# Kernel optimization log

Measured on AMD Instinct MI355X. Metric: run time of the kernel, lower is better.

The kernel has to match this reference:

```python
import jax, jax.numpy as jnp
import numpy as np

GAMMA = 0.03125  # 1/D
REG = 1e-3


def rbf_gram(X, Y, gamma):
    # avoiding the naive [N, M, D] diff tensor from the torch source.
    xx = jnp.sum(X * X, axis=-1)  # [N]
    yy = jnp.sum(Y * Y, axis=-1)  # [M]
    sq = xx[:, None] + yy[None, :] - 2.0 * (X @ Y.T)  # [N, M]
    sq = jnp.maximum(sq, 0.0)
    return jnp.exp(-gamma * sq)


def setup_inputs() -> dict:
    key = jax.random.key(0)
    k1, k2, k3 = jax.random.split(key, 3)
    N, M, D = 8192, 8192, 32
    X_train = jax.random.normal(k1, (N, D), dtype=jnp.float32)
    y_train = jax.random.normal(k2, (N,), dtype=jnp.float32)
    X_test = jax.random.normal(k3, (M, D), dtype=jnp.float32)
    return {"X_train": X_train, "y_train": y_train, "X_test": X_test}


def reference(X_train, y_train, X_test):
    # fit: solve (K + reg * I) alpha = y
    N = X_train.shape[0]
    K = rbf_gram(X_train, X_train, GAMMA)  # [N, N]
    A = K + REG * jnp.eye(N, dtype=K.dtype)
    alpha = jnp.linalg.solve(A, y_train[:, None])[:, 0]  # [N]
    # predict: K_test @ alpha
    K_test = rbf_gram(X_test, X_train, GAMMA)  # [M, N]
    return K_test @ alpha  # [M]
```

## Files before the change

### kernel.cpp

```cpp
#include <hip/hip_runtime.h>


#define NN 8192
#define DD 32
#define REGL 1e-3f
#define NITER 96
#define NBLK 256
#define NC2 (-0.045084220027780106f)
#define SCF (0.3002806023f)

typedef short v8s __attribute__((ext_vector_type(8)));
typedef float v4f __attribute__((ext_vector_type(4)));

__device__ __forceinline__ float fast_exp2(float x) {
#if __has_builtin(__builtin_amdgcn_exp2f)
  return __builtin_amdgcn_exp2f(x);
#else
  float r;
  asm("v_exp_f32 %0, %1" : "=v"(r) : "v"(x));
  return r;
#endif
}

__device__ __forceinline__ float ld_f(const float* p) {
  return __hip_atomic_load(p, __ATOMIC_RELAXED, __HIP_MEMORY_SCOPE_AGENT);
}
__device__ __forceinline__ void st_f(float* p, float v) {
  __hip_atomic_store(p, v, __ATOMIC_RELAXED, __HIP_MEMORY_SCOPE_AGENT);
}
__device__ __forceinline__ double ld_d(const double* p) {
  return __hip_atomic_load(p, __ATOMIC_RELAXED, __HIP_MEMORY_SCOPE_AGENT);
}
__device__ __forceinline__ void st_d(double* p, double v) {
  __hip_atomic_store(p, v, __ATOMIC_RELAXED, __HIP_MEMORY_SCOPE_AGENT);
}

__device__ __forceinline__ ushort f2bf(float x) {
  unsigned u = __float_as_uint(x);
  return (ushort)((u + 0x7fff + ((u >> 16) & 1)) >> 16);
}
__device__ __forceinline__ float bf2f(ushort b) {
  return __uint_as_float(((unsigned)b) << 16);
}

__device__ __forceinline__ double bfly64_d(double v) {
#pragma unroll
  for (int m = 1; m < 64; m <<= 1) v += __shfl_xor(v, m, 64);
  return v;
}
__device__ __forceinline__ double wave_down_sum_d(double v) {
#pragma unroll
  for (int off = 32; off > 0; off >>= 1) v += __shfl_down(v, off, 64);
  return v;
}

__device__ __forceinline__ void gbarrier(unsigned* bar) {
  __builtin_amdgcn_s_waitcnt(0);
  __syncthreads();
  if (threadIdx.x == 0) {
    unsigned* gen = bar + 272;
    unsigned g =
        __hip_atomic_load(gen, __ATOMIC_RELAXED, __HIP_MEMORY_SCOPE_AGENT);
    unsigned a = __hip_atomic_fetch_add(&bar[(blockIdx.x >> 4) * 16], 1u,
                                        __ATOMIC_RELAXED,
                                        __HIP_MEMORY_SCOPE_AGENT);
    bool pub = false;
    if (a == 15u) {
      unsigned ra = __hip_atomic_fetch_add(bar + 256, 1u, __ATOMIC_RELAXED,
                                           __HIP_MEMORY_SCOPE_AGENT);
      if (ra == 15u) {
#pragma unroll
        for (int k = 0; k < 16; ++k)
          __hip_atomic_store(&bar[k * 16], 0u, __ATOMIC_RELAXED,
                             __HIP_MEMORY_SCOPE_AGENT);
        __hip_atomic_store(bar + 256, 0u, __ATOMIC_RELAXED,
                           __HIP_MEMORY_SCOPE_AGENT);
        __builtin_amdgcn_s_waitcnt(0);
        __hip_atomic_store(gen, g + 1u, __ATOMIC_RELAXED,
                           __HIP_MEMORY_SCOPE_AGENT);
        pub = true;
      }
    }
    if (!pub) {
      unsigned t = 0;
      while (__hip_atomic_load(gen, __ATOMIC_RELAXED,
                               __HIP_MEMORY_SCOPE_AGENT) == g) {
        if (t < 64)
          __builtin_amdgcn_s_sleep(1);
        else
          __builtin_amdgcn_s_sleep(8);
        if (++t > (1u << 20)) break;
      }
    }
  }
  __atomic_signal_fence(__ATOMIC_SEQ_CST);
  __syncthreads();
}

__device__ __forceinline__ void conv_frag(const float* __restrict__ X, int row,
                                          int kb, v8s& h, v8s& l) {
  const float4* rp = (const float4*)(X + (size_t)row * DD + kb);
  float4 f0 = rp[0], f1 = rp[1];
  float f[8] = {f0.x, f0.y, f0.z, f0.w, f1.x, f1.y, f1.z, f1.w};
  union {
    v8s v;
    ushort u[8];
  } H, L;
#pragma unroll
  for (int j = 0; j < 8; ++j) {
    float fs = SCF * f[j];
    ushort hb = f2bf(fs);
    H.u[j] = hb;
    L.u[j] = f2bf(fs - bf2f(hb));
  }
  h = H.v;
  l = L.v;
}


__global__ void setup_zero(unsigned* __restrict__ bar) {
  int i = blockIdx.x * 256 + threadIdx.x;
  if (i < 512) bar[i] = 0u;
}

__global__ void row_norms(const float* __restrict__ X, float* __restrict__ xx) {
  int i = blockIdx.x * blockDim.x + threadIdx.x;
  if (i < NN) {
    const float4* row = (const float4*)(X + (size_t)i * DD);
    float s = 0.f;
#pragma unroll
    for (int k = 0; k < DD / 4; ++k) {
      float4 v = row[k];
      s += v.x * v.x + v.y * v.y + v.z * v.z + v.w * v.w;
    }
    xx[i] = NC2 * s;
  }
}

__device__ __forceinline__ void mv_compute(const v8s* ah, const v8s* al,
                                           const ushort (*Bh)[512],
                                           const ushort (*Bl)[512],
                                           const float* Wj, int lane,
                                           float racc[4][4]) {
  const int n = lane & 15;
  for (int t = 0; t < 16; ++t) {
    v8s bh = *(const v8s*)&Bh[t][lane * 8];
    v8s bl = *(const v8s*)&Bl[t][lane * 8];
    float wn = Wj[t * 16 + n];
#pragma unroll
    for (int rs = 0; rs < 4; ++rs) {
      v4f c = {0.f, 0.f, 0.f, 0.f};
      c = __builtin_amdgcn_mfma_f32_16x16x32_bf16(al[rs], bh, c, 0, 0, 0);
      c = __builtin_amdgcn_mfma_f32_16x16x32_bf16(ah[rs], bl, c, 0, 0, 0);
      c = __builtin_amdgcn_mfma_f32_16x16x32_bf16(ah[rs], bh, c, 0, 0, 0);
#pragma unroll
      for (int u = 0; u < 4; ++u)
        racc[rs][u] = fmaf(fast_exp2(c[u]), wn, racc[rs][u]);
    }
  }
}


__global__ __launch_bounds__(1024, 4) void cg_persist(
    const float* __restrict__ Xtr, const float* __restrict__ Xte,
    const float* __restrict__ xx_tr, const float* __restrict__ xx_te,
    const float* __restrict__ y, float* __restrict__ qp0,
    float* __restrict__ qp1, double* __restrict__ rho_s,
    double* __restrict__ mu_s, unsigned* __restrict__ bar,
    float* __restrict__ out, int db) {
  __shared__ __align__(16) ushort Bh[16][512];
  __shared__ __align__(16) ushort Bl[16][512];
  __shared__ float Wj[256];
  __shared__ float Ebj[256];
  __shared__ float Erow[1024];
  __shared__ float Rrow[1024], Qrow[1024];
  __shared__ float Rcol[256], Qcol[256], Pcol[256], Xcol[256];
  __shared__ double sredq[16];
  __shared__ double sredr[16];
  __shared__ float s_ab[2];

  const int tid = threadIdx.x;
  const int lane = tid & 63;
  const int wid = tid >> 6;
  const int n = lane & 15, q4 = lane >> 4;
  const int rbi = blockIdx.x & 7;
  const int sli = blockIdx.x >> 3;
  const int rowbase = rbi * 1024;
  const int i0 = rowbase + wid * 64;
  const int jbase = sli * 256;

  {
    int c = tid & 255;
    int j = jbase + c;
    int g = tid >> 8;
    int tile = c >> 4, cl = c & 15;
    const float4* rp = (const float4*)(Xtr + (size_t)j * DD);
    float4 f0 = rp[2 * g], f1 = rp[2 * g + 1];
    float f[8] = {f0.x, f0.y, f0.z, f0.w, f1.x, f1.y, f1.z, f1.w};
    union {
      ushort u[8];
      uint4 qq;
    } H, L;
#pragma unroll
    for (int e = 0; e < 8; ++e) {
      float fs = SCF * f[e];
      ushort hb = f2bf(fs);
      H.u[e] = hb;
      L.u[e] = f2bf(fs - bf2f(hb));
    }
    int ln = cl + 16 * g;
    *(uint4*)&Bh[tile][ln * 8] = H.qq;
    *(uint4*)&Bl[tile][ln * 8] = L.qq;
  }
  if (tid < 256) Ebj[tid] = fast_exp2(xx_tr[jbase + tid]);
  Erow[tid] = fast_exp2(xx_tr[rowbase + tid]);

  Rrow[tid] = y[rowbase + tid];
  Qrow[tid] = 0.f;
  if (tid < 256) {
    Rcol[tid] = y[jbase + tid];
    Qcol[tid] = 0.f;
    Pcol[tid] = 0.f;
    Xcol[tid] = 0.f;
  }

  v8s ah[4], al[4];
#pragma unroll
  for (int rs = 0; rs < 4; ++rs)
    conv_frag(Xtr, i0 + rs * 16 + n, q4 * 8, ah[rs], al[rs]);

  double rho_old = 1.0, alpha_old = 1.0;
  __syncthreads();

  for (int it = 0; it < NITER; ++it) {
    float* qp = (db && (it & 1)) ? qp1 : qp0;

    if (tid < 256) Wj[tid] = Rcol[tid] * Ebj[tid];
    if (sli == 0) {
      float rvv = Rrow[tid];
      double acc = wave_down_sum_d((double)rvv * (double)rvv);
      if (lane == 0) sredr[wid] = acc;
    }
    __syncthreads();
    if (sli == 0 && tid == 0) {
      double t = 0.0;
#pragma unroll
      for (int k3 = 0; k3 < 16; ++k3) t += sredr[k3];
      st_d(&rho_s[(size_t)it * 128 + rbi * 16], t);
    }

    float racc[4][4] = {};
    mv_compute(ah, al, Bh, Bl, Wj, lane, racc);
#pragma unroll
    for (int rs = 0; rs < 4; ++rs)
#pragma unroll
      for (int u = 0; u < 4; ++u) {
#pragma unroll
        for (int m = 1; m < 16; m <<= 1)
          racc[rs][u] += __shfl_xor(racc[rs][u], m, 64);
      }
    double cmu = 0.0;
    if (n == 0) {
#pragma unroll
      for (int rs = 0; rs < 4; ++rs)
#pragma unroll
        for (int u = 0; u < 4; ++u) {
          int lrow = wid * 64 + rs * 16 + q4 * 4 + u;
          float qc = racc[rs][u] * Erow[lrow];
          st_f(&qp[(size_t)sli * NN + rowbase + lrow], qc);
          cmu += (double)qc * (double)Rrow[lrow];
        }
    }
    cmu = bfly64_d(cmu);
    if (lane == 0) sredq[wid] = cmu;
    __syncthreads();
    if (tid == 0) {
      double t = 0.0;
#pragma unroll
      for (int k3 = 0; k3 < 16; ++k3) t += sredq[k3];
      st_d(&mu_s[(size_t)it * 256 + blockIdx.x], t);
    }

    gbarrier(bar);

    if (wid == 0) {
      const double* mb = mu_s + (size_t)it * 256;
      double m = ld_d(mb + lane) + ld_d(mb + lane + 64) +
                 ld_d(mb + lane + 128) + ld_d(mb + lane + 192);
      double rv_l =
          (lane < 8) ? ld_d(rho_s + (size_t)it * 128 + lane * 16) : 0.0;
      double m1 = bfly64_d(m);
      double r1 = bfly64_d(rv_l);
      double mu = m1 + (double)REGL * r1;
      double beta_d = (it == 0) ? 0.0 : r1 / rho_old;
      double alpha_d =
          (it == 0) ? r1 / mu : r1 / (mu - r1 * beta_d / alpha_old);
      rho_old = r1;
      alpha_old = alpha_d;
      if (lane == 0) {
        s_ab[0] = (float)alpha_d;
        s_ab[1] = (float)beta_d;
      }
    }
    __syncthreads();
    const float alpha = s_ab[0], beta = s_ab[1];

    float wr;
    {
      const float* qb = qp + rowbase + tid;
      float s = 0.f;
#pragma unroll
      for (int s2 = 0; s2 < 32; ++s2) s += ld_f(qb + (size_t)s2 * NN);
      wr = fmaf(REGL, Rrow[tid], s);
    }
    float wc = 0.f;
    if (tid < 256) {
      const float* qb = qp + jbase + tid;
      float s = 0.f;
#pragma unroll
      for (int s2 = 0; s2 < 32; ++s2) s += ld_f(qb + (size_t)s2 * NN);
      wc = fmaf(REGL, Rcol[tid], s);
    }

    {
      float qn = fmaf(beta, Qrow[tid], wr);
      Qrow[tid] = qn;
      Rrow[tid] = fmaf(-alpha, qn, Rrow[tid]);
    }
    if (tid < 256) {
      float qn = fmaf(beta, Qcol[tid], wc);
      Qcol[tid] = qn;
      float pn = fmaf(beta, Pcol[tid], Rcol[tid]);
      Pcol[tid] = pn;
      Xcol[tid] = fmaf(alpha, pn, Xcol[tid]);
      Rcol[tid] = fmaf(-alpha, qn, Rcol[tid]);
    }
    if (!db) gbarrier(bar);
  }

  {
    v8s th[4], tl[4];
#pragma unroll
    for (int rs = 0; rs < 4; ++rs)
      conv_frag(Xte, i0 + rs * 16 + n, q4 * 8, th[rs], tl[rs]);
    if (tid < 256) Wj[tid] = Xcol[tid] * Ebj[tid];
    Erow[tid] = fast_exp2(xx_te[rowbase + tid]);
    __syncthreads();
    float racc[4][4] = {};
    mv_compute(th, tl, Bh, Bl, Wj, lane, racc);
#pragma unroll
    for (int rs = 0; rs < 4; ++rs)
#pragma unroll
      for (int u = 0; u < 4; ++u) {
#pragma unroll
        for (int m = 1; m < 16; m <<= 1)
          racc[rs][u] += __shfl_xor(racc[rs][u], m, 64);
      }
    if (n == 0) {
#pragma unroll
      for (int rs = 0; rs < 4; ++rs)
#pragma unroll
        for (int u = 0; u < 4; ++u) {
          int lrow = wid * 64 + rs * 16 + q4 * 4 + u;
          st_f(&qp0[(size_t)sli * NN + rowbase + lrow],
               racc[rs][u] * Erow[lrow]);
        }
    }
    gbarrier(bar);
    if (sli == 0) {
      const float* qb = qp0 + rowbase + tid;
      float s = 0.f;
#pragma unroll
      for (int s2 = 0; s2 < 32; ++s2) s += ld_f(qb + (size_t)s2 * NN);
      out[rowbase + tid] = s;
    }
  }
}


extern "C" void kernel_launch(void* const* d_in, const int* in_sizes, int n_in,
                              void* d_out, int out_size, void* d_ws,
                              size_t ws_size, hipStream_t stream) {
  const float* X_train = (const float*)d_in[0];
  const float* y_train = (const float*)d_in[1];
  const float* X_test = (const float*)d_in[2];
  float* out = (float*)d_out;

  char* w = (char*)d_ws;
  size_t off = 0;
  float* xx_tr = (float*)(w + off); off += NN * 4;
  float* xx_te = (float*)(w + off); off += NN * 4;
  double* rho_s = (double*)(w + off); off += (size_t)NITER * 128 * 8;
  double* mu_s = (double*)(w + off); off += (size_t)NITER * 256 * 8;
  unsigned* bar = (unsigned*)(w + off); off += 2048;
  off = (off + 255) & ~(size_t)255;
  float* qp0 = (float*)(w + off); off += (size_t)32 * NN * 4;
  size_t need0 = off;
  float* qp1 = (float*)(w + off); off += (size_t)32 * NN * 4;
  size_t need1 = off;

  int db = (ws_size >= need1) ? 1 : 0;
  if (ws_size < need0) return;
  if (!db) qp1 = qp0;

  setup_zero<<<2, 256, 0, stream>>>(bar);
  row_norms<<<NN / 256, 256, 0, stream>>>(X_train, xx_tr);
  row_norms<<<NN / 256, 256, 0, stream>>>(X_test, xx_te);

  cg_persist<<<NBLK, 1024, 0, stream>>>(X_train, X_test, xx_tr, xx_te,
                                        y_train, qp0, qp1, rho_s, mu_s, bar,
                                        out, db);
}
```

Baseline: 2.056 ms.

## Retile persistent CG kernel to square 512x512 blocks over 16x16 grid

Changes the block decomposition of the persistent CG matvec from 1024 rows by 256 columns (8x32 grid) to 512 by 512 (16x16 grid). Each wave now handles 32 rows over 32 column tiles, so per-iteration cross-block partial sums drop from 32 slices to 16 and the post-barrier reduction reads fewer global values. Row and column vector updates are split across the two halves of the thread block so both run concurrently. LDS use for the B fragments doubles, and each wave holds fewer A fragments while making more B loads from LDS.

```diff
diff --git a/kernel.cpp b/kernel.cpp
--- a/kernel.cpp
+++ b/kernel.cpp
@@ -6,6 +6,10 @@
 #define REGL 1e-3f
 #define NITER 96
 #define NBLK 256
+#define NSL 16
+#define NRB 16
+#define ROWS 512
+#define COLS 512
 #define NC2 (-0.045084220027780106f)
 #define SCF (0.3002806023f)
 
@@ -141,14 +145,14 @@
                                            const ushort (*Bh)[512],
                                            const ushort (*Bl)[512],
                                            const float* Wj, int lane,
-                                           float racc[4][4]) {
+                                           float racc[2][4]) {
   const int n = lane & 15;
-  for (int t = 0; t < 16; ++t) {
+  for (int t = 0; t < 32; ++t) {
     v8s bh = *(const v8s*)&Bh[t][lane * 8];
     v8s bl = *(const v8s*)&Bl[t][lane * 8];
     float wn = Wj[t * 16 + n];
 #pragma unroll
-    for (int rs = 0; rs < 4; ++rs) {
+    for (int rs = 0; rs < 2; ++rs) {
       v4f c = {0.f, 0.f, 0.f, 0.f};
       c = __builtin_amdgcn_mfma_f32_16x16x32_bf16(al[rs], bh, c, 0, 0, 0);
       c = __builtin_amdgcn_mfma_f32_16x16x32_bf16(ah[rs], bl, c, 0, 0, 0);
@@ -168,13 +172,13 @@
     float* __restrict__ qp1, double* __restrict__ rho_s,
     double* __restrict__ mu_s, unsigned* __restrict__ bar,
     float* __restrict__ out, int db) {
-  __shared__ __align__(16) ushort Bh[16][512];
-  __shared__ __align__(16) ushort Bl[16][512];
-  __shared__ float Wj[256];
-  __shared__ float Ebj[256];
-  __shared__ float Erow[1024];
-  __shared__ float Rrow[1024], Qrow[1024];
-  __shared__ float Rcol[256], Qcol[256], Pcol[256], Xcol[256];
+  __shared__ __align__(16) ushort Bh[32][512];
+  __shared__ __align__(16) ushort Bl[32][512];
+  __shared__ float Wj[512];
+  __shared__ float Ebj[512];
+  __shared__ float Erow[512];
+  __shared__ float Rrow[512], Qrow[512];
+  __shared__ float Rcol[512], Qcol[512], Pcol[512], Xcol[512];
   __shared__ double sredq[16];
   __shared__ double sredr[16];
   __shared__ float s_ab[2];
@@ -183,19 +187,20 @@
   const int lane = tid & 63;
   const int wid = tid >> 6;
   const int n = lane & 15, q4 = lane >> 4;
-  const int rbi = blockIdx.x & 7;
-  const int sli = blockIdx.x >> 3;
-  const int rowbase = rbi * 1024;
-  const int i0 = rowbase + wid * 64;
-  const int jbase = sli * 256;
-
-  {
-    int c = tid & 255;
+  const int rbi = blockIdx.x & 15;
+  const int sli = blockIdx.x >> 4;
+  const int rowbase = rbi * ROWS;
+  const int i0 = rowbase + wid * 32;
+  const int jbase = sli * COLS;
+
+#pragma unroll
+  for (int rep = 0; rep < 2; ++rep) {
+    int idx = rep * 1024 + tid;
+    int c = idx & 511;
+    int g = idx >> 9;
     int j = jbase + c;
-    int g = tid >> 8;
-    int tile = c >> 4, cl = c & 15;
-    const float4* rp = (const float4*)(Xtr + (size_t)j * DD);
-    float4 f0 = rp[2 * g], f1 = rp[2 * g + 1];
+    const float4* rp = (const float4*)(Xtr + (size_t)j * DD + g * 8);
+    float4 f0 = rp[0], f1 = rp[1];
     float f[8] = {f0.x, f0.y, f0.z, f0.w, f1.x, f1.y, f1.z, f1.w};
     union {
       ushort u[8];
@@ -208,25 +213,25 @@
       H.u[e] = hb;
       L.u[e] = f2bf(fs - bf2f(hb));
     }
+    int tile = c >> 4, cl = c & 15;
     int ln = cl + 16 * g;
     *(uint4*)&Bh[tile][ln * 8] = H.qq;
     *(uint4*)&Bl[tile][ln * 8] = L.qq;
   }
-  if (tid < 256) Ebj[tid] = fast_exp2(xx_tr[jbase + tid]);
-  Erow[tid] = fast_exp2(xx_tr[rowbase + tid]);
-
-  Rrow[tid] = y[rowbase + tid];
-  Qrow[tid] = 0.f;
-  if (tid < 256) {
+  if (tid < 512) {
+    Ebj[tid] = fast_exp2(xx_tr[jbase + tid]);
+    Erow[tid] = fast_exp2(xx_tr[rowbase + tid]);
+    Rrow[tid] = y[rowbase + tid];
+    Qrow[tid] = 0.f;
     Rcol[tid] = y[jbase + tid];
     Qcol[tid] = 0.f;
     Pcol[tid] = 0.f;
     Xcol[tid] = 0.f;
   }
 
-  v8s ah[4], al[4];
-#pragma unroll
-  for (int rs = 0; rs < 4; ++rs)
+  v8s ah[2], al[2];
+#pragma unroll
+  for (int rs = 0; rs < 2; ++rs)
     conv_frag(Xtr, i0 + rs * 16 + n, q4 * 8, ah[rs], al[rs]);
 
   double rho_old = 1.0, alpha_old = 1.0;
@@ -235,9 +240,12 @@
   for (int it = 0; it < NITER; ++it) {
     float* qp = (db && (it & 1)) ? qp1 : qp0;
 
-    if (tid < 256) Wj[tid] = Rcol[tid] * Ebj[tid];
+    if (tid >= 512) {
+      int ct = tid - 512;
+      Wj[ct] = Rcol[ct] * Ebj[ct];
+    }
     if (sli == 0) {
-      float rvv = Rrow[tid];
+      float rvv = (tid < 512) ? Rrow[tid] : 0.f;
       double acc = wave_down_sum_d((double)rvv * (double)rvv);
       if (lane == 0) sredr[wid] = acc;
     }
@@ -246,13 +254,13 @@
       double t = 0.0;
 #pragma unroll
       for (int k3 = 0; k3 < 16; ++k3) t += sredr[k3];
-      st_d(&rho_s[(size_t)it * 128 + rbi * 16], t);
-    }
-
-    float racc[4][4] = {};
+      st_d(&rho_s[(size_t)it * 256 + rbi * 16], t);
+    }
+
+    float racc[2][4] = {};
     mv_compute(ah, al, Bh, Bl, Wj, lane, racc);
 #pragma unroll
-    for (int rs = 0; rs < 4; ++rs)
+    for (int rs = 0; rs < 2; ++rs)
 #pragma unroll
       for (int u = 0; u < 4; ++u) {
 #pragma unroll
@@ -262,10 +270,10 @@
     double cmu = 0.0;
     if (n == 0) {
 #pragma unroll
-      for (int rs = 0; rs < 4; ++rs)
+      for (int rs = 0; rs < 2; ++rs)
 #pragma unroll
         for (int u = 0; u < 4; ++u) {
-          int lrow = wid * 64 + rs * 16 + q4 * 4 + u;
+          int lrow = wid * 32 + rs * 16 + q4 * 4 + u;
           float qc = racc[rs][u] * Erow[lrow];
           st_f(&qp[(size_t)sli * NN + rowbase + lrow], qc);
           cmu += (double)qc * (double)Rrow[lrow];
@@ -288,7 +296,7 @@
       double m = ld_d(mb + lane) + ld_d(mb + lane + 64) +
                  ld_d(mb + lane + 128) + ld_d(mb + lane + 192);
       double rv_l =
-          (lane < 8) ? ld_d(rho_s + (size_t)it * 128 + lane * 16) : 0.0;
+          (lane < 16) ? ld_d(rho_s + (size_t)it * 256 + lane * 16) : 0.0;
       double m1 = bfly64_d(m);
       double r1 = bfly64_d(rv_l);
       double mu = m1 + (double)REGL * r1;
@@ -305,51 +313,48 @@
     __syncthreads();
     const float alpha = s_ab[0], beta = s_ab[1];
 
-    float wr;
-    {
+    if (tid < 512) {
       const float* qb = qp + rowbase + tid;
       float s = 0.f;
 #pragma unroll
-      for (int s2 = 0; s2 < 32; ++s2) s += ld_f(qb + (size_t)s2 * NN);
-      wr = fmaf(REGL, Rrow[tid], s);
-    }
-    float wc = 0.f;
-    if (tid < 256) {
-      const float* qb = qp + jbase + tid;
-      float s = 0.f;
-#pragma unroll
-      for (int s2 = 0; s2 < 32; ++s2) s += ld_f(qb + (size_t)s2 * NN);
-      wc = fmaf(REGL, Rcol[tid], s);
-    }
-
-    {
+      for (int s2 = 0; s2 < NSL; ++s2) s += ld_f(qb + (size_t)s2 * NN);
+      float wr = fmaf(REGL, Rrow[tid], s);
       float qn = fmaf(beta, Qrow[tid], wr);
       Qrow[tid] = qn;
       Rrow[tid] = fmaf(-alpha, qn, Rrow[tid]);
-    }
-    if (tid < 256) {
-      float qn = fmaf(beta, Qcol[tid], wc);
-      Qcol[tid] = qn;
-      float pn = fmaf(beta, Pcol[tid], Rcol[tid]);
-      Pcol[tid] = pn;
-      Xcol[tid] = fmaf(alpha, pn, Xcol[tid]);
-      Rcol[tid] = fmaf(-alpha, qn, Rcol[tid]);
+    } else {
+      int ct = tid - 512;
+      const float* qb = qp + jbase + ct;
+      float s = 0.f;
+#pragma unroll
+      for (int s2 = 0; s2 < NSL; ++s2) s += ld_f(qb + (size_t)s2 * NN);
+      float wc = fmaf(REGL, Rcol[ct], s);
+      float qn = fmaf(beta, Qcol[ct], wc);
+      Qcol[ct] = qn;
+      float pn = fmaf(beta, Pcol[ct], Rcol[ct]);
+      Pcol[ct] = pn;
+      Xcol[ct] = fmaf(alpha, pn, Xcol[ct]);
+      Rcol[ct] = fmaf(-alpha, qn, Rcol[ct]);
     }
     if (!db) gbarrier(bar);
   }
 
   {
-    v8s th[4], tl[4];
-#pragma unroll
-    for (int rs = 0; rs < 4; ++rs)
+    v8s th[2], tl[2];
+#pragma unroll
+    for (int rs = 0; rs < 2; ++rs)
       conv_frag(Xte, i0 + rs * 16 + n, q4 * 8, th[rs], tl[rs]);
-    if (tid < 256) Wj[tid] = Xcol[tid] * Ebj[tid];
-    Erow[tid] = fast_exp2(xx_te[rowbase + tid]);
+    if (tid >= 512) {
+      int ct = tid - 512;
+      Wj[ct] = Xcol[ct] * Ebj[ct];
+    } else {
+      Erow[tid] = fast_exp2(xx_te[rowbase + tid]);
+    }
     __syncthreads();
-    float racc[4][4] = {};
+    float racc[2][4] = {};
     mv_compute(th, tl, Bh, Bl, Wj, lane, racc);
 #pragma unroll
-    for (int rs = 0; rs < 4; ++rs)
+    for (int rs = 0; rs < 2; ++rs)
 #pragma unroll
       for (int u = 0; u < 4; ++u) {
 #pragma unroll
@@ -358,20 +363,20 @@
       }
     if (n == 0) {
 #pragma unroll
-      for (int rs = 0; rs < 4; ++rs)
+      for (int rs = 0; rs < 2; ++rs)
 #pragma unroll
         for (int u = 0; u < 4; ++u) {
-          int lrow = wid * 64 + rs * 16 + q4 * 4 + u;
+          int lrow = wid * 32 + rs * 16 + q4 * 4 + u;
           st_f(&qp0[(size_t)sli * NN + rowbase + lrow],
                racc[rs][u] * Erow[lrow]);
         }
     }
     gbarrier(bar);
-    if (sli == 0) {
+    if (sli == 0 && tid < 512) {
       const float* qb = qp0 + rowbase + tid;
       float s = 0.f;
 #pragma unroll
-      for (int s2 = 0; s2 < 32; ++s2) s += ld_f(qb + (size_t)s2 * NN);
+      for (int s2 = 0; s2 < NSL; ++s2) s += ld_f(qb + (size_t)s2 * NN);
       out[rowbase + tid] = s;
     }
   }
@@ -390,13 +395,13 @@
   size_t off = 0;
   float* xx_tr = (float*)(w + off); off += NN * 4;
   float* xx_te = (float*)(w + off); off += NN * 4;
-  double* rho_s = (double*)(w + off); off += (size_t)NITER * 128 * 8;
+  double* rho_s = (double*)(w + off); off += (size_t)NITER * 256 * 8;
   double* mu_s = (double*)(w + off); off += (size_t)NITER * 256 * 8;
   unsigned* bar = (unsigned*)(w + off); off += 2048;
   off = (off + 255) & ~(size_t)255;
-  float* qp0 = (float*)(w + off); off += (size_t)32 * NN * 4;
+  float* qp0 = (float*)(w + off); off += (size_t)NSL * NN * 4;
   size_t need0 = off;
-  float* qp1 = (float*)(w + off); off += (size_t)32 * NN * 4;
+  float* qp1 = (float*)(w + off); off += (size_t)NSL * NN * 4;
   size_t need1 = off;
 
   int db = (ws_size >= need1) ? 1 : 0;
```

Result: faster. 1.832 ms (-10.9%).
